# Kernel tuning notes

Measured on AMD Instinct MI355X. Metric: run time of the kernel, lower is better.

## Reference

```python
import jax, jax.numpy as jnp
import numpy as np

D = 512        # d_model
DFF = 2048     # d_ffn
H = 8          # n_heads
L = 4          # n_blocks
EPS = 1e-5     # nn.LayerNorm default eps
NEG = -1e9


def _layer_norm(x, g, b):
    m = jnp.mean(x, axis=-1, keepdims=True)
    v = jnp.var(x, axis=-1, keepdims=True)
    return (x - m) / jnp.sqrt(v + EPS) * g + b


def setup_inputs() -> dict:
    key = jax.random.key(0)
    ks = jax.random.split(key, 6)
    B, S = 2, 2048
    s = 0.02
    x = jax.random.normal(ks[0], (B, S, D), dtype=jnp.float32)
    Wq = jax.random.normal(ks[1], (L, D, D), dtype=jnp.float32) * s
    Wk = jax.random.normal(ks[2], (L, D, D), dtype=jnp.float32) * s
    Wv = jax.random.normal(ks[3], (L, D, D), dtype=jnp.float32) * s
    W1 = jax.random.normal(ks[4], (L, D, DFF), dtype=jnp.float32) * s
    W2 = jax.random.normal(ks[5], (L, DFF, D), dtype=jnp.float32) * s
    z_d = jnp.zeros((L, D), dtype=jnp.float32)
    o_d = jnp.ones((L, D), dtype=jnp.float32)
    return {
        'x': x,
        'Wq': Wq, 'bq': z_d, 'Wk': Wk, 'bk': z_d, 'Wv': Wv, 'bv': z_d,
        'W1': W1, 'b1': jnp.zeros((L, DFF), dtype=jnp.float32),
        'W2': W2, 'b2': z_d,
        'g1': o_d, 'beta1': z_d, 'g2': o_d, 'beta2': z_d,
    }


def reference(x, Wq, bq, Wk, bk, Wv, bv, W1, b1, W2, b2, g1, beta1, g2, beta2):
    B, S, Dm = x.shape
    dk = Dm // H
    scale = 1.0 / (dk ** 0.5)

    def block(h, p):
        wq, bq_, wk, bk_, wv, bv_, w1, b1_, w2, b2_, g1_, be1, g2_, be2 = p
        # QKV projections, split heads: [B,S,D] -> [B,H,S,dk]
        q = (h @ wq + bq_).reshape(B, S, H, dk).transpose(0, 2, 1, 3)
        k = (h @ wk + bk_).reshape(B, S, H, dk).transpose(0, 2, 1, 3)
        v = (h @ wv + bv_).reshape(B, S, H, dk).transpose(0, 2, 1, 3)
        scores = jnp.einsum('bhqd,bhkd->bhqk', q, k) * scale
        # original quirk: padding=0, scores exactly equal to 0 get masked to -1e9
        scores = jnp.where(scores != 0, scores, NEG)
        probs = jax.nn.softmax(scores, axis=-1)
        attn = jnp.einsum('bhqk,bhkd->bhqd', probs, v)
        attn = attn.transpose(0, 2, 1, 3).reshape(B, S, Dm)
        h = _layer_norm(attn + h, g1_, be1)           # add_and_norm1
        ff = jax.nn.relu(h @ w1 + b1_) @ w2 + b2_     # position-wise FFN
        h = _layer_norm(h + ff, g2_, be2)             # add_and_norm2
        return h, None

    params = (Wq, bq, Wk, bk, Wv, bv, W1, b1, W2, b2, g1, beta1, g2, beta2)
    out, _ = jax.lax.scan(block, x, params)
    return out
```

## Files before the change

### kernel.cpp

```cpp
#include <hip/hip_runtime.h>
#include <stdint.h>
#include <math.h>


typedef __bf16 bf16_t;
typedef bf16_t bf16x8 __attribute__((ext_vector_type(8)));
typedef bf16_t bf16x4v __attribute__((ext_vector_type(4)));
typedef float  f32x4  __attribute__((ext_vector_type(4)));

__device__ __forceinline__ f32x4 mfma16(bf16x8 a, bf16x8 b, f32x4 c) {
    return __builtin_amdgcn_mfma_f32_16x16x32_bf16(a, b, c, 0, 0, 0);
}

__device__ __forceinline__ void cp16(const void* g, const void* l) {
    auto gp = reinterpret_cast<const __attribute__((address_space(1))) char*>(
        reinterpret_cast<uintptr_t>(g));
    auto lp = reinterpret_cast<__attribute__((address_space(3))) char*>(
        static_cast<uint32_t>(reinterpret_cast<uintptr_t>(l)));
    __builtin_amdgcn_global_load_lds((const __attribute__((address_space(1))) void*)gp,
                                     (__attribute__((address_space(3))) void*)lp,
                                     16, 0, 0);
}

__global__ void wconv_kernel(const float* __restrict__ Wq, const float* __restrict__ Wk,
                             const float* __restrict__ Wv, const float* __restrict__ W1,
                             const float* __restrict__ W2,
                             bf16_t* __restrict__ oQKV, bf16_t* __restrict__ oW1,
                             bf16_t* __restrict__ oW2)
{
    const int l = blockIdx.y;
    int t = blockIdx.x;
    const float* in; bf16_t* out; int Kd, Nd, tt;
    if (t < 192) {
        int m = t / 64; tt = t % 64; Kd = 512; Nd = 512;
        in  = (m == 0 ? Wq : m == 1 ? Wk : Wv) + (size_t)l * 512 * 512;
        out = oQKV + (size_t)l * 1536 * 512 + (size_t)m * 512 * 512;
    } else if (t < 448) {
        tt = t - 192; Kd = 512; Nd = 2048;
        in  = W1 + (size_t)l * 512 * 2048;
        out = oW1 + (size_t)l * 2048 * 512;
    } else {
        tt = t - 448; Kd = 2048; Nd = 512;
        in  = W2 + (size_t)l * 2048 * 512;
        out = oW2 + (size_t)l * 512 * 2048;
    }
    const int ntx = Nd >> 6;
    const int bk = (tt / ntx) * 64, bn = (tt % ntx) * 64;
    __shared__ float tile[64][65];
    const int tid = threadIdx.x;
    #pragma unroll
    for (int i = 0; i < 16; ++i) {
        int idx = i * 256 + tid; int r = idx >> 6, c = idx & 63;
        tile[r][c] = in[(size_t)(bk + r) * Nd + bn + c];
    }
    __syncthreads();
    #pragma unroll
    for (int i = 0; i < 4; ++i) {
        int idx = i * 256 + tid; int n = idx >> 4, kc = (idx & 15) * 4;
        bf16x4v o;
        o[0] = (bf16_t)tile[kc + 0][n];
        o[1] = (bf16_t)tile[kc + 1][n];
        o[2] = (bf16_t)tile[kc + 2][n];
        o[3] = (bf16_t)tile[kc + 3][n];
        *(bf16x4v*)&out[(size_t)(bn + n) * Kd + bk + kc] = o;
    }
}

__global__ void f2b_kernel(const float* __restrict__ in, bf16_t* __restrict__ out, int n)
{
    int i = (blockIdx.x * 256 + threadIdx.x) * 8;
    if (i >= n) return;
    float4 a = *(const float4*)(in + i);
    float4 b = *(const float4*)(in + i + 4);
    bf16x8 o;
    o[0] = (bf16_t)a.x; o[1] = (bf16_t)a.y; o[2] = (bf16_t)a.z; o[3] = (bf16_t)a.w;
    o[4] = (bf16_t)b.x; o[5] = (bf16_t)b.y; o[6] = (bf16_t)b.z; o[7] = (bf16_t)b.w;
    *(bf16x8*)(out + i) = o;
}

template<int MODE, bool RELU>
__global__ __launch_bounds__(256, 2) void gemm_kernel(
    const bf16_t* __restrict__ A, const bf16_t* __restrict__ Wt,
    const float* __restrict__ b0, const float* __restrict__ b1, const float* __restrict__ b2,
    void* __restrict__ o0, void* __restrict__ o1, void* __restrict__ o2,
    int N, int lda, int klen)
{
    __shared__ __align__(16) bf16_t lA[128 * 32];
    __shared__ __align__(16) bf16_t lB[128 * 32];
    const int tid = threadIdx.x;
    const int lane = tid & 63, w = tid >> 6;
    const int wm = w >> 1, wn = w & 1;
    const int l15 = lane & 15, quad = lane >> 4;
    const int row0 = blockIdx.y * 128, col0 = blockIdx.x * 128;
    const int kst = blockIdx.z * klen;
    const int wbase = (tid & 192) * 16;

    f32x4 acc[4][4] = {};
    const char* Ab = (const char*)A;
    const char* Bb = (const char*)Wt;

    for (int k0 = kst; k0 < kst + klen; k0 += 32) {
        __syncthreads();
        #pragma unroll
        for (int p = 0; p < 2; ++p) {
            int o = (p * 256 + tid) * 16;
            int r = o >> 6, cb = o & 63;
            cp16(Ab + ((size_t)(row0 + r) * lda + k0) * 2 + cb, (char*)lA + p * 4096 + wbase);
        }
        #pragma unroll
        for (int p = 0; p < 2; ++p) {
            int o = (p * 256 + tid) * 16;
            int r = o >> 6, cb = o & 63;
            cp16(Bb + ((size_t)(col0 + r) * lda + k0) * 2 + cb, (char*)lB + p * 4096 + wbase);
        }
        __syncthreads();
        bf16x8 af[4], bv_[4];
        #pragma unroll
        for (int i = 0; i < 4; ++i)
            af[i] = *(const bf16x8*)&lA[(wm * 64 + i * 16 + l15) * 32 + quad * 8];
        #pragma unroll
        for (int i = 0; i < 4; ++i)
            bv_[i] = *(const bf16x8*)&lB[(wn * 64 + i * 16 + l15) * 32 + quad * 8];
        #pragma unroll
        for (int mi = 0; mi < 4; ++mi)
            #pragma unroll
            for (int ni = 0; ni < 4; ++ni)
                acc[mi][ni] = mfma16(af[mi], bv_[ni], acc[mi][ni]);
    }

    #pragma unroll
    for (int mi = 0; mi < 4; ++mi) {
        const int rowb = row0 + wm * 64 + mi * 16 + quad * 4;
        #pragma unroll
        for (int ni = 0; ni < 4; ++ni) {
            const int col = col0 + wn * 64 + ni * 16 + l15;
            if (MODE == 1) {
                const float bias = b0[col];
                #pragma unroll
                for (int r = 0; r < 4; ++r) {
                    float v = acc[mi][ni][r] + bias;
                    if (RELU) v = fmaxf(v, 0.f);
                    ((bf16_t*)o0)[(size_t)(rowb + r) * N + col] = (bf16_t)v;
                }
            } else if (MODE == 3) {
                bf16_t* op = (bf16_t*)o0 + (size_t)blockIdx.z * 4096 * 512;
                #pragma unroll
                for (int r = 0; r < 4; ++r)
                    op[(size_t)(rowb + r) * N + col] = (bf16_t)acc[mi][ni][r];
            } else {
                if (col < 512) {
                    const float bias = b0[col];
                    #pragma unroll
                    for (int r = 0; r < 4; ++r)
                        ((bf16_t*)o0)[(size_t)(rowb + r) * 512 + col] =
                            (bf16_t)((acc[mi][ni][r] + bias) * 0.125f);
                } else if (col < 1024) {
                    const int c = col - 512;
                    const float bias = b1[c];
                    #pragma unroll
                    for (int r = 0; r < 4; ++r)
                        ((bf16_t*)o1)[(size_t)(rowb + r) * 512 + c] =
                            (bf16_t)(acc[mi][ni][r] + bias);
                } else {
                    const int cv = col - 1024;
                    const int hh = cv >> 6, d = cv & 63;
                    const float bias = b2[cv];
                    const int b_ = rowb >> 11, s = rowb & 2047;
                    bf16x4v pk;
                    #pragma unroll
                    for (int r = 0; r < 4; ++r)
                        pk[r] = (bf16_t)(acc[mi][ni][r] + bias);
                    *(bf16x4v*)&((bf16_t*)o2)[(size_t)((b_ * 8 + hh) * 64 + d) * 2048 + s] = pk;
                }
            }
        }
    }
}

__global__ __launch_bounds__(256, 7) void attn_kernel(
    const bf16_t* __restrict__ Q, const bf16_t* __restrict__ Kg,
    const bf16_t* __restrict__ Vt, bf16_t* __restrict__ Op,
    float* __restrict__ Lb)
{
    __shared__ __align__(16) bf16_t lK[2][64 * 32];
    __shared__ __align__(16) bf16_t lV[2][64 * 32];
    __shared__ __align__(16) bf16_t lP[4][576];
    const int tid = threadIdx.x;
    const int lane = tid & 63, w = tid >> 6;
    const int l15 = lane & 15, quad = lane >> 4;
    const int bh = blockIdx.y, b = bh >> 3, h = bh & 7;
    const int q0 = blockIdx.x * 64;
    const int sp = blockIdx.z, kbase = sp * 512;
    const int wbase = w * 1024;
    const int srow = tid >> 2, scb = (tid & 3) * 16;

    bf16x8 qf[2];
    #pragma unroll
    for (int ks = 0; ks < 2; ++ks)
        qf[ks] = *(const bf16x8*)&Q[(size_t)(b * 2048 + q0 + w * 16 + l15) * 512
                                     + h * 64 + ks * 32 + quad * 8];

    f32x4 oacc[4] = {};
    float tsum[4] = {0.f, 0.f, 0.f, 0.f};

    for (int t = 0; t < 8; ++t) {
        const int k0 = kbase + t * 64;
        __syncthreads();
        #pragma unroll
        for (int ks = 0; ks < 2; ++ks)
            cp16((const char*)Kg + ((size_t)(b * 2048 + k0 + srow) * 512 + h * 64 + ks * 32) * 2 + scb,
                 (char*)lK[ks] + wbase);
        #pragma unroll
        for (int g = 0; g < 2; ++g)
            cp16((const char*)Vt + ((size_t)(bh * 64 + srow) * 2048 + k0 + g * 32) * 2 + scb,
                 (char*)lV[g] + wbase);
        __syncthreads();

        f32x4 sacc[4] = {};
        #pragma unroll
        for (int ni = 0; ni < 4; ++ni)
            #pragma unroll
            for (int ks = 0; ks < 2; ++ks) {
                bf16x8 kf = *(const bf16x8*)&lK[ks][(ni * 16 + l15) * 32 + quad * 8];
                sacc[ni] = mfma16(qf[ks], kf, sacc[ni]);
            }

        #pragma unroll
        for (int ni = 0; ni < 4; ++ni)
            #pragma unroll
            for (int r = 0; r < 4; ++r) {
                float s = sacc[ni][r];
                float p_ = (s == 0.f) ? 0.f : __expf(s);
                sacc[ni][r] = p_;
                tsum[r] += p_;
            }

        #pragma unroll
        for (int kc = 0; kc < 2; ++kc) {
            #pragma unroll
            for (int nn = 0; nn < 2; ++nn) {
                const int ni = kc * 2 + nn;
                #pragma unroll
                for (int r = 0; r < 4; ++r)
                    lP[w][(quad * 4 + r) * 36 + nn * 16 + l15] = (bf16_t)sacc[ni][r];
            }
            bf16x4v p0 = *(const bf16x4v*)&lP[w][l15 * 36 + quad * 8];
            bf16x4v p1 = *(const bf16x4v*)&lP[w][l15 * 36 + quad * 8 + 4];
            bf16x8 pf;
            #pragma unroll
            for (int j = 0; j < 4; ++j) { pf[j] = p0[j]; pf[4 + j] = p1[j]; }
            #pragma unroll
            for (int nd = 0; nd < 4; ++nd) {
                bf16x8 vf = *(const bf16x8*)&lV[kc][(nd * 16 + l15) * 32 + quad * 8];
                oacc[nd] = mfma16(pf, vf, oacc[nd]);
            }
        }
    }

    #pragma unroll
    for (int r = 0; r < 4; ++r) {
        float s_ = tsum[r];
        s_ += __shfl_xor(s_, 1);
        s_ += __shfl_xor(s_, 2);
        s_ += __shfl_xor(s_, 4);
        s_ += __shfl_xor(s_, 8);
        tsum[r] = s_;
    }

    bf16_t* op = Op + (size_t)sp * 4096 * 512;
    #pragma unroll
    for (int nd = 0; nd < 4; ++nd)
        #pragma unroll
        for (int r = 0; r < 4; ++r) {
            int row = b * 2048 + q0 + w * 16 + quad * 4 + r;
            int col = h * 64 + nd * 16 + l15;
            op[(size_t)row * 512 + col] = (bf16_t)oacc[nd][r];
        }
    if (l15 == 0) {
        #pragma unroll
        for (int r = 0; r < 4; ++r) {
            int row = b * 2048 + q0 + w * 16 + quad * 4 + r;
            Lb[((size_t)row * 8 + h) * 4 + sp] = tsum[r];
        }
    }
}

__global__ void lnadd_c(const bf16_t* __restrict__ Op, const float* __restrict__ Lb,
                        const float* __restrict__ hin,
                        const float* __restrict__ g, const float* __restrict__ be,
                        float* __restrict__ Yf, bf16_t* __restrict__ Yb)
{
    const int row = blockIdx.x * 4 + (threadIdx.x >> 6);
    const int lane = threadIdx.x & 63;
    float v[8]; float s = 0.f;
    #pragma unroll
    for (int i = 0; i < 8; ++i) {
        const int col = lane + i * 64;
        const float4 l4 = *(const float4*)&Lb[((size_t)row * 8 + i) * 4];
        const float inv = 1.f / (l4.x + l4.y + l4.z + l4.w);
        const size_t idx = (size_t)row * 512 + col;
        float o = (float)Op[idx]
                + (float)Op[idx + 2097152]
                + (float)Op[idx + 2 * 2097152]
                + (float)Op[idx + 3 * 2097152];
        v[i] = o * inv + hin[idx];
        s += v[i];
    }
    #pragma unroll
    for (int off = 32; off >= 1; off >>= 1) s += __shfl_xor(s, off);
    const float mean = s * (1.f / 512.f);
    float vs = 0.f;
    #pragma unroll
    for (int i = 0; i < 8; ++i) { float d = v[i] - mean; vs += d * d; }
    #pragma unroll
    for (int off = 32; off >= 1; off >>= 1) vs += __shfl_xor(vs, off);
    const float inv = rsqrtf(vs * (1.f / 512.f) + 1e-5f);
    #pragma unroll
    for (int i = 0; i < 8; ++i) {
        const int c = lane + i * 64;
        const float y = (v[i] - mean) * inv * g[c] + be[c];
        Yf[(size_t)row * 512 + c] = y;
        Yb[(size_t)row * 512 + c] = (bf16_t)y;
    }
}

__global__ void lnadd_f(const bf16_t* __restrict__ G, const float* __restrict__ bias,
                        const float* __restrict__ hres, const float* __restrict__ g,
                        const float* __restrict__ be,
                        float* __restrict__ Yf, bf16_t* __restrict__ Yb)
{
    const int row = blockIdx.x * 4 + (threadIdx.x >> 6);
    const int lane = threadIdx.x & 63;
    float v[8]; float s = 0.f;
    #pragma unroll
    for (int i = 0; i < 8; ++i) {
        const int col = lane + i * 64;
        const size_t idx = (size_t)row * 512 + col;
        float o = (float)G[idx] + (float)G[idx + 2097152]
                + (float)G[idx + 2 * 2097152] + (float)G[idx + 3 * 2097152];
        v[i] = o + bias[col] + hres[idx];
        s += v[i];
    }
    #pragma unroll
    for (int off = 32; off >= 1; off >>= 1) s += __shfl_xor(s, off);
    const float mean = s * (1.f / 512.f);
    float vs = 0.f;
    #pragma unroll
    for (int i = 0; i < 8; ++i) { float d = v[i] - mean; vs += d * d; }
    #pragma unroll
    for (int off = 32; off >= 1; off >>= 1) vs += __shfl_xor(vs, off);
    const float inv = rsqrtf(vs * (1.f / 512.f) + 1e-5f);
    #pragma unroll
    for (int i = 0; i < 8; ++i) {
        const int c = lane + i * 64;
        const float y = (v[i] - mean) * inv * g[c] + be[c];
        Yf[(size_t)row * 512 + c] = y;
        Yb[(size_t)row * 512 + c] = (bf16_t)y;
    }
}

extern "C" void kernel_launch(void* const* d_in, const int* in_sizes, int n_in,
                              void* d_out, int out_size, void* d_ws, size_t ws_size,
                              hipStream_t stream)
{
    const float* x   = (const float*)d_in[0];
    const float* Wq  = (const float*)d_in[1];
    const float* bq  = (const float*)d_in[2];
    const float* Wk  = (const float*)d_in[3];
    const float* bk  = (const float*)d_in[4];
    const float* Wv  = (const float*)d_in[5];
    const float* bv  = (const float*)d_in[6];
    const float* W1  = (const float*)d_in[7];
    const float* b1  = (const float*)d_in[8];
    const float* W2  = (const float*)d_in[9];
    const float* b2  = (const float*)d_in[10];
    const float* g1  = (const float*)d_in[11];
    const float* be1 = (const float*)d_in[12];
    const float* g2  = (const float*)d_in[13];
    const float* be2 = (const float*)d_in[14];

    char* p = (char*)d_ws;
    auto carve = [&](size_t bytes) { char* r = p; p += (bytes + 255) & ~(size_t)255; return r; };
    bf16_t* wQKV = (bf16_t*)carve(4UL * 1536 * 512 * 2);
    bf16_t* wW1t = (bf16_t*)carve(4UL * 2048 * 512 * 2);
    bf16_t* wW2t = (bf16_t*)carve(4UL * 512 * 2048 * 2);
    bf16_t* hbf  = (bf16_t*)carve(4096UL * 512 * 2);
    bf16_t* h2b  = (bf16_t*)carve(4096UL * 512 * 2);
    bf16_t* Fb   = (bf16_t*)carve(4096UL * 2048 * 2);
    bf16_t* R2   = (bf16_t*)carve(4UL * 4096 * 512 * 2);
    float*  Lbuf = (float*)carve(4096UL * 8 * 4 * 4);
    float*  h2f  = (float*)carve(4096UL * 512 * 4);
    float*  hf   = (float*)carve(4096UL * 512 * 4);
    bf16_t* Qb  = Fb;
    bf16_t* Kb  = Fb + 4096UL * 512;
    bf16_t* Vtb = Fb + 2UL * 4096 * 512;

    wconv_kernel<<<dim3(704, 4), 256, 0, stream>>>(Wq, Wk, Wv, W1, W2, wQKV, wW1t, wW2t);
    f2b_kernel<<<dim3(1024), 256, 0, stream>>>(x, hbf, 4096 * 512);

    const float* hin = x;
    for (int l = 0; l < 4; ++l) {
        gemm_kernel<2, false><<<dim3(12, 32, 1), 256, 0, stream>>>(
            hbf, wQKV + (size_t)l * 1536 * 512,
            bq + l * 512, bk + l * 512, bv + l * 512,
            Qb, Kb, Vtb, 1536, 512, 512);
        attn_kernel<<<dim3(32, 16, 4), 256, 0, stream>>>(Qb, Kb, Vtb, R2, Lbuf);
        lnadd_c<<<dim3(1024), 256, 0, stream>>>(R2, Lbuf, hin,
                                                g1 + l * 512, be1 + l * 512, h2f, h2b);
        gemm_kernel<1, true><<<dim3(16, 32, 1), 256, 0, stream>>>(
            h2b, wW1t + (size_t)l * 2048 * 512,
            b1 + l * 2048, nullptr, nullptr,
            Fb, nullptr, nullptr, 2048, 512, 512);
        gemm_kernel<3, false><<<dim3(4, 32, 4), 256, 0, stream>>>(
            Fb, wW2t + (size_t)l * 512 * 2048,
            nullptr, nullptr, nullptr,
            R2, nullptr, nullptr, 512, 2048, 512);
        float* yout = (l == 3) ? (float*)d_out : hf;
        lnadd_f<<<dim3(1024), 256, 0, stream>>>(R2, b2 + l * 512, h2f,
                                                g2 + l * 512, be2 + l * 512, yout, hbf);
        hin = hf;
    }
    (void)in_sizes; (void)n_in; (void)out_size; (void)ws_size;
}
```

Baseline: 543.8 us.

## Double-buffer GEMM and attention LDS loads, vectorize LayerNorm kernels, use exp2 softmax

The GEMM and attention kernels now use double-buffered LDS tiles, issuing the next K-step's global-to-LDS copies before computing the current one, with a single barrier per iteration. This hides load latency, but the larger LDS footprint changes the occupancy hints. The Q scale folds in log2(e) so attention can use exp2f. The PV MFMA is transposed so the output can be written as packed bf16x4. Both LayerNorm kernels switch to contiguous 8-element-per-lane vector loads and stores.

```diff
diff --git a/kernel.cpp b/kernel.cpp
--- a/kernel.cpp
+++ b/kernel.cpp
@@ -79,48 +79,50 @@
 }
 
 template<int MODE, bool RELU>
-__global__ __launch_bounds__(256, 2) void gemm_kernel(
+__global__ __launch_bounds__(256, 3) void gemm_kernel(
     const bf16_t* __restrict__ A, const bf16_t* __restrict__ Wt,
     const float* __restrict__ b0, const float* __restrict__ b1, const float* __restrict__ b2,
     void* __restrict__ o0, void* __restrict__ o1, void* __restrict__ o2,
     int N, int lda, int klen)
 {
-    __shared__ __align__(16) bf16_t lA[128 * 32];
-    __shared__ __align__(16) bf16_t lB[128 * 32];
+    __shared__ __align__(16) bf16_t lA[2][128 * 32];
+    __shared__ __align__(16) bf16_t lB[2][128 * 32];
     const int tid = threadIdx.x;
     const int lane = tid & 63, w = tid >> 6;
     const int wm = w >> 1, wn = w & 1;
     const int l15 = lane & 15, quad = lane >> 4;
     const int row0 = blockIdx.y * 128, col0 = blockIdx.x * 128;
-    const int kst = blockIdx.z * klen;
+    const int kst = blockIdx.z * klen, kend = kst + klen;
     const int wbase = (tid & 192) * 16;
 
     f32x4 acc[4][4] = {};
     const char* Ab = (const char*)A;
     const char* Bb = (const char*)Wt;
 
-    for (int k0 = kst; k0 < kst + klen; k0 += 32) {
-        __syncthreads();
+    auto stage = [&](int k0, int buf) {
         #pragma unroll
         for (int p = 0; p < 2; ++p) {
             int o = (p * 256 + tid) * 16;
             int r = o >> 6, cb = o & 63;
-            cp16(Ab + ((size_t)(row0 + r) * lda + k0) * 2 + cb, (char*)lA + p * 4096 + wbase);
-        }
-        #pragma unroll
-        for (int p = 0; p < 2; ++p) {
-            int o = (p * 256 + tid) * 16;
-            int r = o >> 6, cb = o & 63;
-            cp16(Bb + ((size_t)(col0 + r) * lda + k0) * 2 + cb, (char*)lB + p * 4096 + wbase);
-        }
+            cp16(Ab + ((size_t)(row0 + r) * lda + k0) * 2 + cb, (char*)lA[buf] + p * 4096 + wbase);
+            cp16(Bb + ((size_t)(col0 + r) * lda + k0) * 2 + cb, (char*)lB[buf] + p * 4096 + wbase);
+        }
+    };
+
+    stage(kst, 0);
+    int it = 0;
+    for (int k0 = kst; k0 < kend; k0 += 32, ++it) {
         __syncthreads();
+        if (k0 + 32 < kend) stage(k0 + 32, (it + 1) & 1);
+        const bf16_t* cA = lA[it & 1];
+        const bf16_t* cB = lB[it & 1];
         bf16x8 af[4], bv_[4];
         #pragma unroll
         for (int i = 0; i < 4; ++i)
-            af[i] = *(const bf16x8*)&lA[(wm * 64 + i * 16 + l15) * 32 + quad * 8];
+            af[i] = *(const bf16x8*)&cA[(wm * 64 + i * 16 + l15) * 32 + quad * 8];
         #pragma unroll
         for (int i = 0; i < 4; ++i)
-            bv_[i] = *(const bf16x8*)&lB[(wn * 64 + i * 16 + l15) * 32 + quad * 8];
+            bv_[i] = *(const bf16x8*)&cB[(wn * 64 + i * 16 + l15) * 32 + quad * 8];
         #pragma unroll
         for (int mi = 0; mi < 4; ++mi)
             #pragma unroll
@@ -153,7 +155,7 @@
                     #pragma unroll
                     for (int r = 0; r < 4; ++r)
                         ((bf16_t*)o0)[(size_t)(rowb + r) * 512 + col] =
-                            (bf16_t)((acc[mi][ni][r] + bias) * 0.125f);
+                            (bf16_t)((acc[mi][ni][r] + bias) * 0.18033688f);
                 } else if (col < 1024) {
                     const int c = col - 512;
                     const float bias = b1[c];
@@ -177,13 +179,13 @@
     }
 }
 
-__global__ __launch_bounds__(256, 7) void attn_kernel(
+__global__ __launch_bounds__(256, 4) void attn_kernel(
     const bf16_t* __restrict__ Q, const bf16_t* __restrict__ Kg,
     const bf16_t* __restrict__ Vt, bf16_t* __restrict__ Op,
     float* __restrict__ Lb)
 {
-    __shared__ __align__(16) bf16_t lK[2][64 * 32];
-    __shared__ __align__(16) bf16_t lV[2][64 * 32];
+    __shared__ __align__(16) bf16_t lK[2][2][64 * 32];
+    __shared__ __align__(16) bf16_t lV[2][2][64 * 32];
     __shared__ __align__(16) bf16_t lP[4][576];
     const int tid = threadIdx.x;
     const int lane = tid & 63, w = tid >> 6;
@@ -194,49 +196,57 @@
     const int wbase = w * 1024;
     const int srow = tid >> 2, scb = (tid & 3) * 16;
 
+    auto stageKV = [&](int k0, int buf) {
+        #pragma unroll
+        for (int ks = 0; ks < 2; ++ks)
+            cp16((const char*)Kg + ((size_t)(b * 2048 + k0 + srow) * 512 + h * 64 + ks * 32) * 2 + scb,
+                 (char*)lK[buf][ks] + wbase);
+        #pragma unroll
+        for (int g = 0; g < 2; ++g)
+            cp16((const char*)Vt + ((size_t)(bh * 64 + srow) * 2048 + k0 + g * 32) * 2 + scb,
+                 (char*)lV[buf][g] + wbase);
+    };
+
     bf16x8 qf[2];
     #pragma unroll
     for (int ks = 0; ks < 2; ++ks)
         qf[ks] = *(const bf16x8*)&Q[(size_t)(b * 2048 + q0 + w * 16 + l15) * 512
                                      + h * 64 + ks * 32 + quad * 8];
 
-    f32x4 oacc[4] = {};
+    f32x4 oaccT[4] = {};
     float tsum[4] = {0.f, 0.f, 0.f, 0.f};
 
+    stageKV(kbase, 0);
     for (int t = 0; t < 8; ++t) {
-        const int k0 = kbase + t * 64;
         __syncthreads();
-        #pragma unroll
-        for (int ks = 0; ks < 2; ++ks)
-            cp16((const char*)Kg + ((size_t)(b * 2048 + k0 + srow) * 512 + h * 64 + ks * 32) * 2 + scb,
-                 (char*)lK[ks] + wbase);
-        #pragma unroll
-        for (int g = 0; g < 2; ++g)
-            cp16((const char*)Vt + ((size_t)(bh * 64 + srow) * 2048 + k0 + g * 32) * 2 + scb,
-                 (char*)lV[g] + wbase);
-        __syncthreads();
+        if (t < 7) stageKV(kbase + (t + 1) * 64, (t + 1) & 1);
+        const bf16_t* cK0 = lK[t & 1][0];
+        const bf16_t* cK1 = lK[t & 1][1];
+        const bf16_t* cV0 = lV[t & 1][0];
+        const bf16_t* cV1 = lV[t & 1][1];
 
         f32x4 sacc[4] = {};
         #pragma unroll
-        for (int ni = 0; ni < 4; ++ni)
-            #pragma unroll
-            for (int ks = 0; ks < 2; ++ks) {
-                bf16x8 kf = *(const bf16x8*)&lK[ks][(ni * 16 + l15) * 32 + quad * 8];
-                sacc[ni] = mfma16(qf[ks], kf, sacc[ni]);
-            }
+        for (int ni = 0; ni < 4; ++ni) {
+            bf16x8 kf0 = *(const bf16x8*)&cK0[(ni * 16 + l15) * 32 + quad * 8];
+            bf16x8 kf1 = *(const bf16x8*)&cK1[(ni * 16 + l15) * 32 + quad * 8];
+            sacc[ni] = mfma16(qf[0], kf0, sacc[ni]);
+            sacc[ni] = mfma16(qf[1], kf1, sacc[ni]);
+        }
 
         #pragma unroll
         for (int ni = 0; ni < 4; ++ni)
             #pragma unroll
             for (int r = 0; r < 4; ++r) {
                 float s = sacc[ni][r];
-                float p_ = (s == 0.f) ? 0.f : __expf(s);
+                float p_ = (s == 0.f) ? 0.f : exp2f(s);
                 sacc[ni][r] = p_;
                 tsum[r] += p_;
             }
 
         #pragma unroll
         for (int kc = 0; kc < 2; ++kc) {
+            const bf16_t* cV = (kc == 0) ? cV0 : cV1;
             #pragma unroll
             for (int nn = 0; nn < 2; ++nn) {
                 const int ni = kc * 2 + nn;
@@ -251,8 +261,8 @@
             for (int j = 0; j < 4; ++j) { pf[j] = p0[j]; pf[4 + j] = p1[j]; }
             #pragma unroll
             for (int nd = 0; nd < 4; ++nd) {
-                bf16x8 vf = *(const bf16x8*)&lV[kc][(nd * 16 + l15) * 32 + quad * 8];
-                oacc[nd] = mfma16(pf, vf, oacc[nd]);
+                bf16x8 vf = *(const bf16x8*)&cV[(nd * 16 + l15) * 32 + quad * 8];
+                oaccT[nd] = mfma16(vf, pf, oaccT[nd]);
             }
         }
     }
@@ -268,14 +278,16 @@
     }
 
     bf16_t* op = Op + (size_t)sp * 4096 * 512;
-    #pragma unroll
-    for (int nd = 0; nd < 4; ++nd)
-        #pragma unroll
-        for (int r = 0; r < 4; ++r) {
-            int row = b * 2048 + q0 + w * 16 + quad * 4 + r;
-            int col = h * 64 + nd * 16 + l15;
-            op[(size_t)row * 512 + col] = (bf16_t)oacc[nd][r];
-        }
+    {
+        const int row = b * 2048 + q0 + w * 16 + l15;
+        #pragma unroll
+        for (int nd = 0; nd < 4; ++nd) {
+            bf16x4v pk;
+            #pragma unroll
+            for (int r = 0; r < 4; ++r) pk[r] = (bf16_t)oaccT[nd][r];
+            *(bf16x4v*)&op[(size_t)row * 512 + h * 64 + nd * 16 + quad * 4] = pk;
+        }
+    }
     if (l15 == 0) {
         #pragma unroll
         for (int r = 0; r < 4; ++r) {
@@ -292,36 +304,46 @@
 {
     const int row = blockIdx.x * 4 + (threadIdx.x >> 6);
     const int lane = threadIdx.x & 63;
+    const int c0 = lane * 8;
+    const int head = lane >> 3;
+    const float4 l4 = *(const float4*)&Lb[((size_t)row * 8 + head) * 4];
+    const float linv = 1.f / (l4.x + l4.y + l4.z + l4.w);
+    const size_t idx = (size_t)row * 512 + c0;
+    bf16x8 o0 = *(const bf16x8*)&Op[idx];
+    bf16x8 o1 = *(const bf16x8*)&Op[idx + 2097152];
+    bf16x8 o2 = *(const bf16x8*)&Op[idx + 2 * 2097152];
+    bf16x8 o3 = *(const bf16x8*)&Op[idx + 3 * 2097152];
+    float4 h0 = *(const float4*)&hin[idx];
+    float4 h1 = *(const float4*)&hin[idx + 4];
+    const float hr[8] = {h0.x, h0.y, h0.z, h0.w, h1.x, h1.y, h1.z, h1.w};
     float v[8]; float s = 0.f;
     #pragma unroll
-    for (int i = 0; i < 8; ++i) {
-        const int col = lane + i * 64;
-        const float4 l4 = *(const float4*)&Lb[((size_t)row * 8 + i) * 4];
-        const float inv = 1.f / (l4.x + l4.y + l4.z + l4.w);
-        const size_t idx = (size_t)row * 512 + col;
-        float o = (float)Op[idx]
-                + (float)Op[idx + 2097152]
-                + (float)Op[idx + 2 * 2097152]
-                + (float)Op[idx + 3 * 2097152];
-        v[i] = o * inv + hin[idx];
-        s += v[i];
+    for (int j = 0; j < 8; ++j) {
+        v[j] = ((float)o0[j] + (float)o1[j] + (float)o2[j] + (float)o3[j]) * linv + hr[j];
+        s += v[j];
     }
     #pragma unroll
     for (int off = 32; off >= 1; off >>= 1) s += __shfl_xor(s, off);
     const float mean = s * (1.f / 512.f);
     float vs = 0.f;
     #pragma unroll
-    for (int i = 0; i < 8; ++i) { float d = v[i] - mean; vs += d * d; }
+    for (int j = 0; j < 8; ++j) { float d = v[j] - mean; vs += d * d; }
     #pragma unroll
     for (int off = 32; off >= 1; off >>= 1) vs += __shfl_xor(vs, off);
     const float inv = rsqrtf(vs * (1.f / 512.f) + 1e-5f);
-    #pragma unroll
-    for (int i = 0; i < 8; ++i) {
-        const int c = lane + i * 64;
-        const float y = (v[i] - mean) * inv * g[c] + be[c];
-        Yf[(size_t)row * 512 + c] = y;
-        Yb[(size_t)row * 512 + c] = (bf16_t)y;
-    }
+    float4 g0 = *(const float4*)&g[c0], g1 = *(const float4*)&g[c0 + 4];
+    float4 b0 = *(const float4*)&be[c0], b1 = *(const float4*)&be[c0 + 4];
+    const float gg[8] = {g0.x, g0.y, g0.z, g0.w, g1.x, g1.y, g1.z, g1.w};
+    const float bb[8] = {b0.x, b0.y, b0.z, b0.w, b1.x, b1.y, b1.z, b1.w};
+    float y[8]; bf16x8 yb;
+    #pragma unroll
+    for (int j = 0; j < 8; ++j) {
+        y[j] = (v[j] - mean) * inv * gg[j] + bb[j];
+        yb[j] = (bf16_t)y[j];
+    }
+    *(float4*)&Yf[idx]     = make_float4(y[0], y[1], y[2], y[3]);
+    *(float4*)&Yf[idx + 4] = make_float4(y[4], y[5], y[6], y[7]);
+    *(bf16x8*)&Yb[idx] = yb;
 }
 
 __global__ void lnadd_f(const bf16_t* __restrict__ G, const float* __restrict__ bias,
@@ -331,32 +353,45 @@
 {
     const int row = blockIdx.x * 4 + (threadIdx.x >> 6);
     const int lane = threadIdx.x & 63;
+    const int c0 = lane * 8;
+    const size_t idx = (size_t)row * 512 + c0;
+    bf16x8 o0 = *(const bf16x8*)&G[idx];
+    bf16x8 o1 = *(const bf16x8*)&G[idx + 2097152];
+    bf16x8 o2 = *(const bf16x8*)&G[idx + 2 * 2097152];
+    bf16x8 o3 = *(const bf16x8*)&G[idx + 3 * 2097152];
+    float4 h0 = *(const float4*)&hres[idx];
+    float4 h1 = *(const float4*)&hres[idx + 4];
+    float4 bi0 = *(const float4*)&bias[c0], bi1 = *(const float4*)&bias[c0 + 4];
+    const float hr[8] = {h0.x, h0.y, h0.z, h0.w, h1.x, h1.y, h1.z, h1.w};
+    const float bs[8] = {bi0.x, bi0.y, bi0.z, bi0.w, bi1.x, bi1.y, bi1.z, bi1.w};
     float v[8]; float s = 0.f;
     #pragma unroll
-    for (int i = 0; i < 8; ++i) {
-        const int col = lane + i * 64;
-        const size_t idx = (size_t)row * 512 + col;
-        float o = (float)G[idx] + (float)G[idx + 2097152]
-                + (float)G[idx + 2 * 2097152] + (float)G[idx + 3 * 2097152];
-        v[i] = o + bias[col] + hres[idx];
-        s += v[i];
+    for (int j = 0; j < 8; ++j) {
+        v[j] = (float)o0[j] + (float)o1[j] + (float)o2[j] + (float)o3[j] + bs[j] + hr[j];
+        s += v[j];
     }
     #pragma unroll
     for (int off = 32; off >= 1; off >>= 1) s += __shfl_xor(s, off);
     const float mean = s * (1.f / 512.f);
     float vs = 0.f;
     #pragma unroll
-    for (int i = 0; i < 8; ++i) { float d = v[i] - mean; vs += d * d; }
+    for (int j = 0; j < 8; ++j) { float d = v[j] - mean; vs += d * d; }
     #pragma unroll
     for (int off = 32; off >= 1; off >>= 1) vs += __shfl_xor(vs, off);
     const float inv = rsqrtf(vs * (1.f / 512.f) + 1e-5f);
-    #pragma unroll
-    for (int i = 0; i < 8; ++i) {
-        const int c = lane + i * 64;
-        const float y = (v[i] - mean) * inv * g[c] + be[c];
-        Yf[(size_t)row * 512 + c] = y;
-        Yb[(size_t)row * 512 + c] = (bf16_t)y;
-    }
+    float4 g0 = *(const float4*)&g[c0], g1 = *(const float4*)&g[c0 + 4];
+    float4 b0 = *(const float4*)&be[c0], b1 = *(const float4*)&be[c0 + 4];
+    const float gg[8] = {g0.x, g0.y, g0.z, g0.w, g1.x, g1.y, g1.z, g1.w};
+    const float bb[8] = {b0.x, b0.y, b0.z, b0.w, b1.x, b1.y, b1.z, b1.w};
+    float y[8]; bf16x8 yb;
+    #pragma unroll
+    for (int j = 0; j < 8; ++j) {
+        y[j] = (v[j] - mean) * inv * gg[j] + bb[j];
+        yb[j] = (bf16_t)y[j];
+    }
+    *(float4*)&Yf[idx]     = make_float4(y[0], y[1], y[2], y[3]);
+    *(float4*)&Yf[idx + 4] = make_float4(y[4], y[5], y[6], y[7]);
+    *(bf16x8*)&Yb[idx] = yb;
 }
 
 extern "C" void kernel_launch(void* const* d_in, const int* in_sizes, int n_in,
```

New measurement: 531.8 us. 2.2% less time.
